# Kernel tuning notes

Hardware: AMD Instinct MI355X
Metric: run time of the kernel (lower is better)

## Reference

```python
import jax, jax.numpy as jnp
import numpy as np

H = 256          # hidden_dim from config
B, S = 128, 2048 # batch, seq_len
D_CTX, D_RFX = 6, 2


def setup_inputs() -> dict:
    key = jax.random.key(0)
    ks = jax.random.split(key, 16)
    def lin(k, out_d, in_d):
        # torch nn.Linear default init: U(-1/sqrt(in_d), 1/sqrt(in_d))
        bound = 1.0 / np.sqrt(in_d)
        k1, k2 = jax.random.split(k)
        w = jax.random.uniform(k1, (out_d, in_d), jnp.float32, -bound, bound)
        b = jax.random.uniform(k2, (out_d,), jnp.float32, -bound, bound)
        return w, b
    x = jax.random.normal(ks[0], (B, S, D_CTX), jnp.float32)
    # GRUCell params (torch layout: rows ordered [reset, update, new])
    bnd = 1.0 / np.sqrt(H)
    w_ih = jax.random.uniform(ks[1], (3 * H, D_CTX), jnp.float32, -bnd, bnd)
    w_hh = jax.random.uniform(ks[2], (3 * H, H), jnp.float32, -bnd, bnd)
    b_ih = jax.random.uniform(ks[3], (3 * H,), jnp.float32, -bnd, bnd)
    b_hh = jax.random.uniform(ks[4], (3 * H,), jnp.float32, -bnd, bnd)
    w_gain, b_gain = lin(ks[5], D_RFX, H)
    w_bias, b_bias = lin(ks[6], 4, H)
    w_reflex, b_reflex = lin(ks[7], H, D_RFX)
    w_policy, b_policy = lin(ks[8], 2, H)
    w_motor, b_motor = lin(ks[9], 2, H)
    return dict(x=x, w_ih=w_ih, w_hh=w_hh, b_ih=b_ih, b_hh=b_hh,
                w_gain=w_gain, b_gain=b_gain, w_bias=w_bias, b_bias=b_bias,
                w_reflex=w_reflex, b_reflex=b_reflex,
                w_policy=w_policy, b_policy=b_policy,
                w_motor=w_motor, b_motor=b_motor)


def _forward(x, w_ih, w_hh, b_ih, b_hh, w_gain, b_gain, w_bias, b_bias,
             w_reflex, b_reflex, w_policy, b_policy, w_motor, b_motor):
    # x_context == cat(x[:,:,0:2], x[:,:,2:3], x[:,:,3:6]) == x itself
    x_reflex = x[:, :, 0:2]
    # Precompute input contribution to all 3 GRU gates: [B, S, 3H]
    gates_x = jnp.einsum('bsd,gd->bsg', x, w_ih) + b_ih
    gates_x_t = jnp.swapaxes(gates_x, 0, 1)     # [S, B, 3H]
    x_reflex_t = jnp.swapaxes(x_reflex, 0, 1)   # [S, B, 2]

    h0 = jnp.zeros((x.shape[0], H), x.dtype)

    def step(h, inp):
        gi, xr = inp
        gh = h @ w_hh.T + b_hh
        r = jax.nn.sigmoid(gi[:, :H] + gh[:, :H])
        z = jax.nn.sigmoid(gi[:, H:2 * H] + gh[:, H:2 * H])
        n = jnp.tanh(gi[:, 2 * H:] + r * gh[:, 2 * H:])
        h_new = (1.0 - z) * n + z * h
        gain = jax.nn.sigmoid(h_new @ w_gain.T + b_gain)   # [B,2]
        bias = h_new @ w_bias.T + b_bias                    # [B,4]
        feat = jax.nn.relu((xr * gain) @ w_reflex.T + b_reflex)  # [B,H]
        probs = feat @ w_policy.T + b_policy + bias[:, 0:2]
        dirs = jnp.tanh(feat @ w_motor.T + b_motor + bias[:, 2:4])
        y = jnp.concatenate([probs, dirs], axis=1)          # [B,4]
        return h_new, (y, h_new)

    _, (y_t, h_t) = jax.lax.scan(step, h0, (gates_x_t, x_reflex_t))
    y_pred = jnp.swapaxes(y_t, 0, 1)          # [B,S,4]
    router_activity = jnp.swapaxes(h_t, 0, 1) # [B,S,H]
    return y_pred, router_activity


def reference(x, w_ih, w_hh, b_ih, b_hh, w_gain, b_gain, w_bias, b_bias,
              w_reflex, b_reflex, w_policy, b_policy, w_motor, b_motor):
    return _forward(x, w_ih, w_hh, b_ih, b_hh, w_gain, b_gain, w_bias, b_bias,
                    w_reflex, b_reflex, w_policy, b_policy, w_motor, b_motor)
```

## Files before the change

kernel.cpp:

```cpp
#include <hip/hip_runtime.h>
#include <cstdint>
#include <cstddef>

#define Hn 256
#define Sn 2048
#define Bn 128
#define NT 1024

typedef _Float16 half2_t __attribute__((ext_vector_type(2)));

__device__ __forceinline__ half2_t bc2_(unsigned int u){ return __builtin_bit_cast(half2_t, u); }

__device__ __forceinline__ float fdot2_(half2_t a, half2_t b, float c){
#if __has_builtin(__builtin_amdgcn_fdot2)
  return __builtin_amdgcn_fdot2(a, b, c, false);
#else
  float d;
  asm volatile("v_dot2_f32_f16 %0, %1, %2, %3" : "=v"(d) : "v"(a), "v"(b), "v"(c));
  return d;
#endif
}

__device__ __forceinline__ float rfl_(float v){
  return __builtin_bit_cast(float, __builtin_amdgcn_readfirstlane(__builtin_bit_cast(int, v)));
}

__device__ __forceinline__ half2_t pkrtz_(float a, float b){
  return __builtin_bit_cast(half2_t, __builtin_amdgcn_cvt_pkrtz(a, b));
}

__device__ __forceinline__ float qsum_(float v){
  int x = __builtin_bit_cast(int, v);
  int y = __builtin_amdgcn_mov_dpp(x, 0xB1, 0xF, 0xF, true);
  v += __builtin_bit_cast(float, y);
  x = __builtin_bit_cast(int, v);
  y = __builtin_amdgcn_mov_dpp(x, 0x4E, 0xF, 0xF, true);
  return v + __builtin_bit_cast(float, y);
}

__device__ __forceinline__ float wsum_(float v){
  int x;
  x = __builtin_amdgcn_update_dpp(0, __builtin_bit_cast(int, v), 0x111, 0xF, 0xF, false);
  v += __builtin_bit_cast(float, x);
  x = __builtin_amdgcn_update_dpp(0, __builtin_bit_cast(int, v), 0x112, 0xF, 0xF, false);
  v += __builtin_bit_cast(float, x);
  x = __builtin_amdgcn_update_dpp(0, __builtin_bit_cast(int, v), 0x114, 0xF, 0xF, false);
  v += __builtin_bit_cast(float, x);
  x = __builtin_amdgcn_update_dpp(0, __builtin_bit_cast(int, v), 0x118, 0xF, 0xF, false);
  v += __builtin_bit_cast(float, x);
  x = __builtin_amdgcn_update_dpp(0, __builtin_bit_cast(int, v), 0x142, 0xA, 0xF, false);
  v += __builtin_bit_cast(float, x);
  x = __builtin_amdgcn_update_dpp(0, __builtin_bit_cast(int, v), 0x143, 0xC, 0xF, false);
  v += __builtin_bit_cast(float, x);
  return v;
}

__device__ __forceinline__ float sigmoid_(float v){ return 1.0f/(1.0f+__expf(-v)); }
__device__ __forceinline__ float tanh_(float v){
  float e = __expf(-2.0f*__builtin_fabsf(v));
  float r = (1.0f-e)/(1.0f+e);
  return __builtin_copysignf(r, v);
}

#define F32_(M) M(0) M(1) M(2) M(3) M(4) M(5) M(6) M(7) M(8) M(9) M(10) M(11) \
  M(12) M(13) M(14) M(15) M(16) M(17) M(18) M(19) M(20) M(21) M(22) M(23) \
  M(24) M(25) M(26) M(27) M(28) M(29) M(30) M(31)

__global__ void __launch_bounds__(NT)
bio_rnn(const float* __restrict__ x,
        const float* __restrict__ w_ih, const float* __restrict__ w_hh,
        const float* __restrict__ b_ih, const float* __restrict__ b_hh,
        const float* __restrict__ w_gain, const float* __restrict__ b_gain,
        const float* __restrict__ w_bias, const float* __restrict__ b_bias,
        const float* __restrict__ w_reflex, const float* __restrict__ b_reflex,
        const float* __restrict__ w_policy, const float* __restrict__ b_policy,
        const float* __restrict__ w_motor, const float* __restrict__ b_motor,
        float* __restrict__ y_out, float* __restrict__ router)
{
  const int b  = blockIdx.x;
  const int t  = threadIdx.x;
  const int kq = t & 3;
  const int j  = t >> 2;

  __shared__ unsigned int WL[NT * 20];
  __shared__ __align__(16) unsigned char hraw[4*160];
  __shared__ float PRE[4][Hn];
  __shared__ float REDp[4][8];
  __shared__ float REDq[4][4];
  __shared__ float HW[13][Hn];
  __shared__ float SB[10];

#define DAG(i) unsigned agr##i, agz##i;
  F32_(DAG)
#undef DAG
  {
    const float* wrR = w_hh + (size_t)(j      )*Hn + kq*64;
    const float* wrZ = w_hh + (size_t)(j + Hn )*Hn + kq*64;
#define WAG(i) { unsigned pr = __builtin_bit_cast(unsigned, pkrtz_(wrR[2*i], wrR[2*i+1])); \
                 unsigned pz = __builtin_bit_cast(unsigned, pkrtz_(wrZ[2*i], wrZ[2*i+1])); \
                 asm("v_accvgpr_write_b32 %0, %1" : "=a"(agr##i) : "v"(pr)); \
                 asm("v_accvgpr_write_b32 %0, %1" : "=a"(agz##i) : "v"(pz)); }
    F32_(WAG)
#undef WAG
  }
  uint4 WR0, WR1, WR2, WR3;
  {
    const float* wrN = w_hh + (size_t)(j + 2*Hn)*Hn + kq*64;
#define PK(m) __builtin_bit_cast(unsigned, pkrtz_(wrN[2*(m)], wrN[2*(m)+1]))
    WR0 = (uint4){PK(0),PK(1),PK(2),PK(3)};
    WR1 = (uint4){PK(4),PK(5),PK(6),PK(7)};
    WR2 = (uint4){PK(8),PK(9),PK(10),PK(11)};
    WR3 = (uint4){PK(12),PK(13),PK(14),PK(15)};
    #pragma unroll
    for (int i = 0; i < 16; i++)
      WL[t*20 + i] = __builtin_bit_cast(unsigned, pkrtz_(wrN[32+2*i], wrN[32+2*i+1]));
#undef PK
  }
  half2_t wi0, wi1, wi2; float bd0, bd1, bd2, bd3;
  {
    half2_t z; z.x=(_Float16)0.f; z.y=(_Float16)0.f;
    wi0=z; wi1=z; wi2=z; bd0=bd1=bd2=bd3=0.f;
    if (kq < 3){
      wi0 = pkrtz_(w_ih[(size_t)(j       )*6+2*kq], w_ih[(size_t)(j       )*6+2*kq+1]);
      wi1 = pkrtz_(w_ih[(size_t)(j +  Hn )*6+2*kq], w_ih[(size_t)(j +  Hn )*6+2*kq+1]);
      wi2 = pkrtz_(w_ih[(size_t)(j + 2*Hn)*6+2*kq], w_ih[(size_t)(j + 2*Hn)*6+2*kq+1]);
    } else {
      bd0 = b_ih[j]      + b_hh[j];
      bd1 = b_ih[j+Hn]   + b_hh[j+Hn];
      bd2 = b_hh[j+2*Hn];
      bd3 = b_ih[j+2*Hn];
    }
  }
  if (t < Hn){
    HW[0][t] = w_gain[t];        HW[1][t]  = w_gain[Hn + t];
    HW[2][t] = w_bias[t];        HW[3][t]  = w_bias[Hn + t];
    HW[4][t] = w_bias[2*Hn + t]; HW[5][t]  = w_bias[3*Hn + t];
    HW[6][t] = w_reflex[2*t];    HW[7][t]  = w_reflex[2*t + 1];
    HW[8][t] = b_reflex[t];
    HW[9][t] = w_policy[t];      HW[10][t] = w_policy[Hn + t];
    HW[11][t] = w_motor[t];      HW[12][t] = w_motor[Hn + t];
  }
  if (t < 160) ((unsigned int*)hraw)[t] = 0u;
  if (t == 0){
    SB[0]=b_gain[0]; SB[1]=b_gain[1];
    SB[2]=b_bias[0]; SB[3]=b_bias[1]; SB[4]=b_bias[2]; SB[5]=b_bias[3];
    SB[6]=b_policy[0]; SB[7]=b_policy[1]; SB[8]=b_motor[0]; SB[9]=b_motor[1];
  }
  float hprev = 0.f;
  __syncthreads();

  const float* xp   = x      + (size_t)b * Sn * 6;
  float* rbase      = router + (size_t)b * Sn * Hn;
  const uint4* hc4  = (const uint4*)(hraw + kq*160);
  const uint4* WLv  = (const uint4*)WL;

#define GCH(c, nv_, r0,r1,r2,r3) { \
    const uint4 Hc = hc4[c]; const uint4 Nw = (nv_); \
    unsigned u0,u1,u2,u3,v0,v1,v2,v3; \
    asm("v_accvgpr_read_b32 %0, %1" : "=v"(u0) : "a"(agr##r0)); \
    asm("v_accvgpr_read_b32 %0, %1" : "=v"(u1) : "a"(agr##r1)); \
    asm("v_accvgpr_read_b32 %0, %1" : "=v"(u2) : "a"(agr##r2)); \
    asm("v_accvgpr_read_b32 %0, %1" : "=v"(u3) : "a"(agr##r3)); \
    asm("v_accvgpr_read_b32 %0, %1" : "=v"(v0) : "a"(agz##r0)); \
    asm("v_accvgpr_read_b32 %0, %1" : "=v"(v1) : "a"(agz##r1)); \
    asm("v_accvgpr_read_b32 %0, %1" : "=v"(v2) : "a"(agz##r2)); \
    asm("v_accvgpr_read_b32 %0, %1" : "=v"(v3) : "a"(agz##r3)); \
    a0=fdot2_(bc2_(u0),bc2_(Hc.x),a0); a1=fdot2_(bc2_(v0),bc2_(Hc.x),a1); a2=fdot2_(bc2_(Nw.x),bc2_(Hc.x),a2); \
    a0=fdot2_(bc2_(u1),bc2_(Hc.y),a0); a1=fdot2_(bc2_(v1),bc2_(Hc.y),a1); a2=fdot2_(bc2_(Nw.y),bc2_(Hc.y),a2); \
    a0=fdot2_(bc2_(u2),bc2_(Hc.z),a0); a1=fdot2_(bc2_(v2),bc2_(Hc.z),a1); a2=fdot2_(bc2_(Nw.z),bc2_(Hc.z),a2); \
    a0=fdot2_(bc2_(u3),bc2_(Hc.w),a0); a1=fdot2_(bc2_(v3),bc2_(Hc.w),a1); a2=fdot2_(bc2_(Nw.w),bc2_(Hc.w),a2); }

  for (int s = 0; s < Sn; s++){
    const float x0=rfl_(xp[0]), x1=rfl_(xp[1]), x2=rfl_(xp[2]);
    const float x3=rfl_(xp[3]), x4=rfl_(xp[4]), x5=rfl_(xp[5]);
    float xa = (kq==0)?x0:((kq==1)?x2:x4);
    float xb = (kq==0)?x1:((kq==1)?x3:x5);
    half2_t xpk = pkrtz_(xa, xb);

    float a0 = fdot2_(wi0, xpk, bd0);
    float a1 = fdot2_(wi1, xpk, bd1);
    float a2 = bd2;
    float a3 = fdot2_(wi2, xpk, bd3);

    const int wlb = t*5;
    GCH(0, WR0,  0, 1, 2, 3)
    GCH(1, WR1,  4, 5, 6, 7)
    GCH(2, WR2,  8, 9,10,11)
    GCH(3, WR3, 12,13,14,15)
    GCH(4, WLv[wlb+0], 16,17,18,19)
    GCH(5, WLv[wlb+1], 20,21,22,23)
    GCH(6, WLv[wlb+2], 24,25,26,27)
    GCH(7, WLv[wlb+3], 28,29,30,31)

    a0 = qsum_(a0); a1 = qsum_(a1); a2 = qsum_(a2); a3 = qsum_(a3);
    if (kq == 0){ PRE[0][j]=a0; PRE[1][j]=a1; PRE[2][j]=a2; PRE[3][j]=a3; }
    __syncthreads();

    if (t < Hn){
      float pr = PRE[0][t], pz = PRE[1][t], pg = PRE[2][t], pn = PRE[3][t];
      float r = sigmoid_(pr);
      float z = sigmoid_(pz);
      float n = tanh_(pn + r*pg);
      float h = (1.f - z)*n + z*hprev;
      hprev = h;
      *(_Float16*)(hraw + (t>>6)*160 + (t&63)*2) = (_Float16)h;
      rbase[(size_t)s*Hn + t] = h;
      float p0 = wsum_(h*HW[0][t]);
      float p1 = wsum_(h*HW[1][t]);
      float p2 = wsum_(h*HW[2][t]);
      float p3 = wsum_(h*HW[3][t]);
      float p4 = wsum_(h*HW[4][t]);
      float p5 = wsum_(h*HW[5][t]);
      if ((t & 63) == 63){
        const int wv = t >> 6;
        REDp[wv][0]=p0; REDp[wv][1]=p1; REDp[wv][2]=p2;
        REDp[wv][3]=p3; REDp[wv][4]=p4; REDp[wv][5]=p5;
      }
    }
    __syncthreads();
    if (t < Hn){
      float g0 = REDp[0][0]+REDp[1][0]+REDp[2][0]+REDp[3][0] + SB[0];
      float g1 = REDp[0][1]+REDp[1][1]+REDp[2][1]+REDp[3][1] + SB[1];
      g0 = sigmoid_(g0); g1 = sigmoid_(g1);
      float f = (x0*g0)*HW[6][t] + (x1*g1)*HW[7][t] + HW[8][t];
      f = fmaxf(f, 0.f);
      float q0 = wsum_(f*HW[9][t]);
      float q1 = wsum_(f*HW[10][t]);
      float q2 = wsum_(f*HW[11][t]);
      float q3 = wsum_(f*HW[12][t]);
      if ((t & 63) == 63){
        const int wv = t >> 6;
        REDq[wv][0]=q0; REDq[wv][1]=q1; REDq[wv][2]=q2; REDq[wv][3]=q3;
      }
    }
    __syncthreads();
    if (t == 0){
      float s0 = REDq[0][0]+REDq[1][0]+REDq[2][0]+REDq[3][0];
      float s1 = REDq[0][1]+REDq[1][1]+REDq[2][1]+REDq[3][1];
      float s2 = REDq[0][2]+REDq[1][2]+REDq[2][2]+REDq[3][2];
      float s3 = REDq[0][3]+REDq[1][3]+REDq[2][3]+REDq[3][3];
      float B0 = REDp[0][2]+REDp[1][2]+REDp[2][2]+REDp[3][2] + SB[2];
      float B1 = REDp[0][3]+REDp[1][3]+REDp[2][3]+REDp[3][3] + SB[3];
      float B2 = REDp[0][4]+REDp[1][4]+REDp[2][4]+REDp[3][4] + SB[4];
      float B3 = REDp[0][5]+REDp[1][5]+REDp[2][5]+REDp[3][5] + SB[5];
      float4 o;
      o.x = s0 + SB[6] + B0;
      o.y = s1 + SB[7] + B1;
      o.z = tanh_(s2 + SB[8] + B2);
      o.w = tanh_(s3 + SB[9] + B3);
      *(float4*)(y_out + (size_t)b * Sn * 4 + (size_t)s * 4) = o;
    }
    xp += 6;
  }
#undef GCH
}

extern "C" void kernel_launch(void* const* d_in, const int* in_sizes, int n_in,
                              void* d_out, int out_size, void* d_ws, size_t ws_size,
                              hipStream_t stream)
{
  const float* x        = (const float*)d_in[0];
  const float* w_ih     = (const float*)d_in[1];
  const float* w_hh     = (const float*)d_in[2];
  const float* b_ih     = (const float*)d_in[3];
  const float* b_hh     = (const float*)d_in[4];
  const float* w_gain   = (const float*)d_in[5];
  const float* b_gain   = (const float*)d_in[6];
  const float* w_bias   = (const float*)d_in[7];
  const float* b_bias   = (const float*)d_in[8];
  const float* w_reflex = (const float*)d_in[9];
  const float* b_reflex = (const float*)d_in[10];
  const float* w_policy = (const float*)d_in[11];
  const float* b_policy = (const float*)d_in[12];
  const float* w_motor  = (const float*)d_in[13];
  const float* b_motor  = (const float*)d_in[14];

  float* y_out  = (float*)d_out;
  float* router = (float*)d_out + (size_t)Bn * Sn * 4;

  bio_rnn<<<dim3(Bn), dim3(NT), 0, stream>>>(
      x, w_ih, w_hh, b_ih, b_hh, w_gain, b_gain, w_bias, b_bias,
      w_reflex, b_reflex, w_policy, b_policy, w_motor, b_motor,
      y_out, router);
}
```

Measured before the change: 6.467 ms.

## Double-buffer hidden state and defer output heads to rotating wavefront

Each step now needs one barrier instead of three. Every quad computes the gate nonlinearities redundantly from its own reduced sums, which removes the PRE shared-memory round trip. The hidden state is double-buffered in LDS, so the output heads for step s-1 run in a single wavefront while the next GRU matvec proceeds; that wavefront rotates across the 16 waves and reduces with shuffles. The x input is prefetched one step ahead. The cost is extra redundant transcendental work per thread and an uneven load on whichever wave is computing the heads in a given step.

```diff
diff --git a/kernel.cpp b/kernel.cpp
--- a/kernel.cpp
+++ b/kernel.cpp
@@ -21,10 +21,6 @@
 #endif
 }
 
-__device__ __forceinline__ float rfl_(float v){
-  return __builtin_bit_cast(float, __builtin_amdgcn_readfirstlane(__builtin_bit_cast(int, v)));
-}
-
 __device__ __forceinline__ half2_t pkrtz_(float a, float b){
   return __builtin_bit_cast(half2_t, __builtin_amdgcn_cvt_pkrtz(a, b));
 }
@@ -36,23 +32,6 @@
   x = __builtin_bit_cast(int, v);
   y = __builtin_amdgcn_mov_dpp(x, 0x4E, 0xF, 0xF, true);
   return v + __builtin_bit_cast(float, y);
-}
-
-__device__ __forceinline__ float wsum_(float v){
-  int x;
-  x = __builtin_amdgcn_update_dpp(0, __builtin_bit_cast(int, v), 0x111, 0xF, 0xF, false);
-  v += __builtin_bit_cast(float, x);
-  x = __builtin_amdgcn_update_dpp(0, __builtin_bit_cast(int, v), 0x112, 0xF, 0xF, false);
-  v += __builtin_bit_cast(float, x);
-  x = __builtin_amdgcn_update_dpp(0, __builtin_bit_cast(int, v), 0x114, 0xF, 0xF, false);
-  v += __builtin_bit_cast(float, x);
-  x = __builtin_amdgcn_update_dpp(0, __builtin_bit_cast(int, v), 0x118, 0xF, 0xF, false);
-  v += __builtin_bit_cast(float, x);
-  x = __builtin_amdgcn_update_dpp(0, __builtin_bit_cast(int, v), 0x142, 0xA, 0xF, false);
-  v += __builtin_bit_cast(float, x);
-  x = __builtin_amdgcn_update_dpp(0, __builtin_bit_cast(int, v), 0x143, 0xC, 0xF, false);
-  v += __builtin_bit_cast(float, x);
-  return v;
 }
 
 __device__ __forceinline__ float sigmoid_(float v){ return 1.0f/(1.0f+__expf(-v)); }
@@ -81,12 +60,10 @@
   const int t  = threadIdx.x;
   const int kq = t & 3;
   const int j  = t >> 2;
+  const int l  = t & 63;
 
   __shared__ unsigned int WL[NT * 20];
-  __shared__ __align__(16) unsigned char hraw[4*160];
-  __shared__ float PRE[4][Hn];
-  __shared__ float REDp[4][8];
-  __shared__ float REDq[4][4];
+  __shared__ __align__(16) unsigned char hraw[2*640];
   __shared__ float HW[13][Hn];
   __shared__ float SB[10];
 
@@ -140,7 +117,7 @@
     HW[9][t] = w_policy[t];      HW[10][t] = w_policy[Hn + t];
     HW[11][t] = w_motor[t];      HW[12][t] = w_motor[Hn + t];
   }
-  if (t < 160) ((unsigned int*)hraw)[t] = 0u;
+  if (t < 320) ((unsigned int*)hraw)[t] = 0u;
   if (t == 0){
     SB[0]=b_gain[0]; SB[1]=b_gain[1];
     SB[2]=b_bias[0]; SB[3]=b_bias[1]; SB[4]=b_bias[2]; SB[5]=b_bias[3];
@@ -149,10 +126,61 @@
   float hprev = 0.f;
   __syncthreads();
 
-  const float* xp   = x      + (size_t)b * Sn * 6;
-  float* rbase      = router + (size_t)b * Sn * Hn;
-  const uint4* hc4  = (const uint4*)(hraw + kq*160);
-  const uint4* WLv  = (const uint4*)WL;
+  const float* xg  = x + (size_t)b * Sn * 6;
+  const float* xq  = xg + 2*((kq < 3) ? kq : 0);
+  float* rbase     = router + (size_t)b * Sn * Hn;
+  const uint4* WLv = (const uint4*)WL;
+
+  auto heads = [&](int sprev, const unsigned* hb){
+    const int dw0 = l + ((l >> 5) << 3);
+    unsigned hp0 = hb[dw0];
+    unsigned hp1 = hb[80 + dw0];
+    half2_t h01 = bc2_(hp0), h23 = bc2_(hp1);
+    float h0=(float)h01.x, h1=(float)h01.y, h2=(float)h23.x, h3=(float)h23.y;
+    float p[6];
+    #pragma unroll
+    for (int g = 0; g < 6; g++){
+      float2 wa = *(const float2*)&HW[g][2*l];
+      float2 wb = *(const float2*)&HW[g][128+2*l];
+      p[g] = h0*wa.x + h1*wa.y + h2*wb.x + h3*wb.y;
+    }
+    #pragma unroll
+    for (int off = 32; off >= 1; off >>= 1){
+      p[0]+=__shfl_xor(p[0],off); p[1]+=__shfl_xor(p[1],off); p[2]+=__shfl_xor(p[2],off);
+      p[3]+=__shfl_xor(p[3],off); p[4]+=__shfl_xor(p[4],off); p[5]+=__shfl_xor(p[5],off);
+    }
+    float g0 = sigmoid_(p[0] + SB[0]);
+    float g1 = sigmoid_(p[1] + SB[1]);
+    float2 xr = *(const float2*)(xg + (size_t)sprev*6);
+    float u0 = xr.x * g0, u1 = xr.y * g1;
+    float2 w6a = *(const float2*)&HW[6][2*l], w6b = *(const float2*)&HW[6][128+2*l];
+    float2 w7a = *(const float2*)&HW[7][2*l], w7b = *(const float2*)&HW[7][128+2*l];
+    float2 w8a = *(const float2*)&HW[8][2*l], w8b = *(const float2*)&HW[8][128+2*l];
+    float f0 = fmaxf(u0*w6a.x + u1*w7a.x + w8a.x, 0.f);
+    float f1 = fmaxf(u0*w6a.y + u1*w7a.y + w8a.y, 0.f);
+    float f2 = fmaxf(u0*w6b.x + u1*w7b.x + w8b.x, 0.f);
+    float f3 = fmaxf(u0*w6b.y + u1*w7b.y + w8b.y, 0.f);
+    float q[4];
+    #pragma unroll
+    for (int g = 0; g < 4; g++){
+      float2 wa = *(const float2*)&HW[9+g][2*l];
+      float2 wb = *(const float2*)&HW[9+g][128+2*l];
+      q[g] = f0*wa.x + f1*wa.y + f2*wb.x + f3*wb.y;
+    }
+    #pragma unroll
+    for (int off = 32; off >= 1; off >>= 1){
+      q[0]+=__shfl_xor(q[0],off); q[1]+=__shfl_xor(q[1],off);
+      q[2]+=__shfl_xor(q[2],off); q[3]+=__shfl_xor(q[3],off);
+    }
+    if (l == 0){
+      float4 o;
+      o.x = q[0] + SB[6] + (p[2] + SB[2]);
+      o.y = q[1] + SB[7] + (p[3] + SB[3]);
+      o.z = tanh_(q[2] + SB[8] + (p[4] + SB[4]));
+      o.w = tanh_(q[3] + SB[9] + (p[5] + SB[5]));
+      *(float4*)(y_out + (size_t)b * Sn * 4 + (size_t)sprev * 4) = o;
+    }
+  };
 
 #define GCH(c, nv_, r0,r1,r2,r3) { \
     const uint4 Hc = hc4[c]; const uint4 Nw = (nv_); \
@@ -170,18 +198,25 @@
     a0=fdot2_(bc2_(u2),bc2_(Hc.z),a0); a1=fdot2_(bc2_(v2),bc2_(Hc.z),a1); a2=fdot2_(bc2_(Nw.z),bc2_(Hc.z),a2); \
     a0=fdot2_(bc2_(u3),bc2_(Hc.w),a0); a1=fdot2_(bc2_(v3),bc2_(Hc.w),a1); a2=fdot2_(bc2_(Nw.w),bc2_(Hc.w),a2); }
 
+  float2 px = *(const float2*)xq;
+  unsigned cur = 0;
+
   for (int s = 0; s < Sn; s++){
-    const float x0=rfl_(xp[0]), x1=rfl_(xp[1]), x2=rfl_(xp[2]);
-    const float x3=rfl_(xp[3]), x4=rfl_(xp[4]), x5=rfl_(xp[5]);
-    float xa = (kq==0)?x0:((kq==1)?x2:x4);
-    float xb = (kq==0)?x1:((kq==1)?x3:x5);
-    half2_t xpk = pkrtz_(xa, xb);
+    const unsigned char* hb = hraw + cur*640;
+    unsigned char* hw = hraw + (cur^1)*640;
+
+    if (s > 0 && (t >> 6) == (s & 15)) heads(s-1, (const unsigned*)hb);
+
+    half2_t xpk = pkrtz_(px.x, px.y);
+    if (s + 1 < Sn) px = *(const float2*)(xq + 6);
+    xq += 6;
 
     float a0 = fdot2_(wi0, xpk, bd0);
     float a1 = fdot2_(wi1, xpk, bd1);
     float a2 = bd2;
     float a3 = fdot2_(wi2, xpk, bd3);
 
+    const uint4* hc4 = (const uint4*)(hb + kq*160);
     const int wlb = t*5;
     GCH(0, WR0,  0, 1, 2, 3)
     GCH(1, WR1,  4, 5, 6, 7)
@@ -193,65 +228,20 @@
     GCH(7, WLv[wlb+3], 28,29,30,31)
 
     a0 = qsum_(a0); a1 = qsum_(a1); a2 = qsum_(a2); a3 = qsum_(a3);
-    if (kq == 0){ PRE[0][j]=a0; PRE[1][j]=a1; PRE[2][j]=a2; PRE[3][j]=a3; }
+
+    float r = sigmoid_(a0);
+    float z = sigmoid_(a1);
+    float n = tanh_(a3 + r*a2);
+    float h = (1.f - z)*n + z*hprev;
+    hprev = h;
+    if (kq == 0){
+      *(_Float16*)(hw + (j>>6)*160 + (j&63)*2) = (_Float16)h;
+      rbase[(size_t)s*Hn + j] = h;
+    }
     __syncthreads();
-
-    if (t < Hn){
-      float pr = PRE[0][t], pz = PRE[1][t], pg = PRE[2][t], pn = PRE[3][t];
-      float r = sigmoid_(pr);
-      float z = sigmoid_(pz);
-      float n = tanh_(pn + r*pg);
-      float h = (1.f - z)*n + z*hprev;
-      hprev = h;
-      *(_Float16*)(hraw + (t>>6)*160 + (t&63)*2) = (_Float16)h;
-      rbase[(size_t)s*Hn + t] = h;
-      float p0 = wsum_(h*HW[0][t]);
-      float p1 = wsum_(h*HW[1][t]);
-      float p2 = wsum_(h*HW[2][t]);
-      float p3 = wsum_(h*HW[3][t]);
-      float p4 = wsum_(h*HW[4][t]);
-      float p5 = wsum_(h*HW[5][t]);
-      if ((t & 63) == 63){
-        const int wv = t >> 6;
-        REDp[wv][0]=p0; REDp[wv][1]=p1; REDp[wv][2]=p2;
-        REDp[wv][3]=p3; REDp[wv][4]=p4; REDp[wv][5]=p5;
-      }
-    }
-    __syncthreads();
-    if (t < Hn){
-      float g0 = REDp[0][0]+REDp[1][0]+REDp[2][0]+REDp[3][0] + SB[0];
-      float g1 = REDp[0][1]+REDp[1][1]+REDp[2][1]+REDp[3][1] + SB[1];
-      g0 = sigmoid_(g0); g1 = sigmoid_(g1);
-      float f = (x0*g0)*HW[6][t] + (x1*g1)*HW[7][t] + HW[8][t];
-      f = fmaxf(f, 0.f);
-      float q0 = wsum_(f*HW[9][t]);
-      float q1 = wsum_(f*HW[10][t]);
-      float q2 = wsum_(f*HW[11][t]);
-      float q3 = wsum_(f*HW[12][t]);
-      if ((t & 63) == 63){
-        const int wv = t >> 6;
-        REDq[wv][0]=q0; REDq[wv][1]=q1; REDq[wv][2]=q2; REDq[wv][3]=q3;
-      }
-    }
-    __syncthreads();
-    if (t == 0){
-      float s0 = REDq[0][0]+REDq[1][0]+REDq[2][0]+REDq[3][0];
-      float s1 = REDq[0][1]+REDq[1][1]+REDq[2][1]+REDq[3][1];
-      float s2 = REDq[0][2]+REDq[1][2]+REDq[2][2]+REDq[3][2];
-      float s3 = REDq[0][3]+REDq[1][3]+REDq[2][3]+REDq[3][3];
-      float B0 = REDp[0][2]+REDp[1][2]+REDp[2][2]+REDp[3][2] + SB[2];
-      float B1 = REDp[0][3]+REDp[1][3]+REDp[2][3]+REDp[3][3] + SB[3];
-      float B2 = REDp[0][4]+REDp[1][4]+REDp[2][4]+REDp[3][4] + SB[4];
-      float B3 = REDp[0][5]+REDp[1][5]+REDp[2][5]+REDp[3][5] + SB[5];
-      float4 o;
-      o.x = s0 + SB[6] + B0;
-      o.y = s1 + SB[7] + B1;
-      o.z = tanh_(s2 + SB[8] + B2);
-      o.w = tanh_(s3 + SB[9] + B3);
-      *(float4*)(y_out + (size_t)b * Sn * 4 + (size_t)s * 4) = o;
-    }
-    xp += 6;
-  }
+    cur ^= 1;
+  }
+  if ((t >> 6) == 0) heads(Sn-1, (const unsigned*)(hraw + cur*640));
 #undef GCH
 }
 
```

Result: slower. 9.542 ms (+47.6%).
